# Kernel optimization log

Measured on AMD Instinct MI355X. Metric: run time of the kernel, lower is better.

Reference implementation:

```python
import jax, jax.numpy as jnp
import numpy as np

N = 50000          # nodes
E = 800000         # edges (before self loops)
IN_C = 64
HID = 32
HEADS = 4
HC = HID * HEADS   # 128
OUT_C = 3
NEG_SLOPE = 0.2


def _lin(key, fan_out, fan_in, scale=None):
    if scale is None:
        scale = 1.0 / np.sqrt(fan_in)
    return (jax.random.normal(key, (fan_out, fan_in), dtype=jnp.float32) * scale)


def setup_inputs() -> dict:
    key = jax.random.key(0)
    ks = jax.random.split(key, 24)
    inp = {
        "x": jax.random.normal(ks[0], (N, IN_C), dtype=jnp.float32),
        "edge_index": jax.random.randint(ks[1], (2, E), 0, N, dtype=jnp.int64),
        "edge_attr": jax.random.uniform(ks[2], (E,), dtype=jnp.float32),
        "g1_Wl": _lin(ks[3], HC, IN_C), "g1_bl": jnp.zeros((HC,), jnp.float32),
        "g1_Wr": _lin(ks[4], HC, IN_C), "g1_br": jnp.zeros((HC,), jnp.float32),
        "g1_We": _lin(ks[5], HC, 1),
        "g1_att": jax.random.normal(ks[6], (HEADS, HID), dtype=jnp.float32) / np.sqrt(HID),
        "g1_bias": jnp.zeros((HC,), jnp.float32),
        "g2_Wl": _lin(ks[7], HC, HC), "g2_bl": jnp.zeros((HC,), jnp.float32),
        "g2_Wr": _lin(ks[8], HC, HC), "g2_br": jnp.zeros((HC,), jnp.float32),
        "g2_We": _lin(ks[9], HC, 1),
        "g2_att": jax.random.normal(ks[10], (1, HC), dtype=jnp.float32) / np.sqrt(HC),
        "g2_bias": jnp.zeros((HC,), jnp.float32),
        # residual projection (in_channels != hidden*heads)
        "res1_W": _lin(ks[11], HC, IN_C), "res1_b": jnp.zeros((HC,), jnp.float32),
        # MLP head
        "fc1_W": _lin(ks[12], HID, HC), "fc1_b": jnp.zeros((HID,), jnp.float32),
        "fc2_W": _lin(ks[13], 32, HID), "fc2_b": jnp.zeros((32,), jnp.float32),
        "fc3_W": _lin(ks[14], OUT_C, 32), "fc3_b": jnp.zeros((OUT_C,), jnp.float32),
    }
    return inp


def gatv2_conv(x, src, dst, ea, Wl, bl, Wr, br, We, att, bias, heads, out_c):
    # x: [N, F]; src/dst: [E'] (self loops already appended); ea: [E', 1]
    xl = (x @ Wl.T + bl).reshape(N, heads, out_c)   # lin_l -> source features
    xr = (x @ Wr.T + br).reshape(N, heads, out_c)   # lin_r -> target features
    ee = (ea @ We.T).reshape(-1, heads, out_c)      # lin_edge (no bias)
    xj = xl[src]                                    # [E', H, C] gather
    m = jax.nn.leaky_relu(xj + xr[dst] + ee, NEG_SLOPE)
    alpha = jnp.einsum('ehc,hc->eh', m, att)        # per-edge logits
    amax = jax.ops.segment_max(alpha, dst, num_segments=N)
    ex = jnp.exp(alpha - amax[dst])
    denom = jax.ops.segment_sum(ex, dst, num_segments=N)
    alpha = ex / (denom[dst] + 1e-16)               # segment softmax over incoming edges
    out = jax.ops.segment_sum(xj * alpha[..., None], dst, num_segments=N)
    return out.reshape(N, heads * out_c) + bias


def reference(x, edge_index, edge_attr,
              g1_Wl, g1_bl, g1_Wr, g1_br, g1_We, g1_att, g1_bias,
              g2_Wl, g2_bl, g2_Wr, g2_br, g2_We, g2_att, g2_bias,
              res1_W, res1_b, fc1_W, fc1_b, fc2_W, fc2_b, fc3_W, fc3_b):
    ea = edge_attr.reshape(-1, 1)                   # dim()==1 -> view(-1,1)
    # add self loops; edge_attr fill_value='mean' (PyG default)
    loop = jnp.arange(N)
    src = jnp.concatenate([edge_index[0], loop])
    dst = jnp.concatenate([edge_index[1], loop])
    ea_mean = jnp.mean(ea, axis=0, keepdims=True)
    ea_full = jnp.concatenate([ea, jnp.broadcast_to(ea_mean, (N, 1))], axis=0)

    h = gatv2_conv(x, src, dst, ea_full, g1_Wl, g1_bl, g1_Wr, g1_br,
                   g1_We, g1_att, g1_bias, HEADS, HID)
    h = jax.nn.elu(h + (x @ res1_W.T + res1_b))     # residual (projected) + ELU

    h2 = gatv2_conv(h, src, dst, ea_full, g2_Wl, g2_bl, g2_Wr, g2_br,
                    g2_We, g2_att, g2_bias, 1, HC)
    h2 = jax.nn.elu(h2 + h)                         # identity residual + ELU

    y = jax.nn.relu(h2 @ fc1_W.T + fc1_b)
    y = jax.nn.relu(y @ fc2_W.T + fc2_b)
    return y @ fc3_W.T + fc3_b                      # [N, 3]
```

## Files before the change

kernel.cpp:

```cpp
#include <hip/hip_runtime.h>
#include <math.h>


typedef short s16x8 __attribute__((ext_vector_type(8)));
typedef float f32x4 __attribute__((ext_vector_type(4)));
typedef float f32x2 __attribute__((ext_vector_type(2)));

__device__ inline unsigned short f2bf(float x) {
  unsigned int u = __float_as_uint(x);
  return (unsigned short)((u + 0x7fffu + ((u >> 16) & 1u)) >> 16);
}
__device__ inline float bf2f(unsigned short h) {
  return __uint_as_float(((unsigned int)h) << 16);
}
__device__ inline float bflo(unsigned int u) { return __uint_as_float(u << 16); }
__device__ inline float bfhi(unsigned int u) { return __uint_as_float(u & 0xffff0000u); }

template <int CTRL>
__device__ inline float dpp_addf(float x) {
  int y = __builtin_amdgcn_update_dpp(0, __float_as_int(x), CTRL, 0xf, 0xf, false);
  return x + __int_as_float(y);
}

__global__ __launch_bounds__(256) void prep_hist(
    const float* __restrict__ g1wl, const float* __restrict__ g1wr,
    const float* __restrict__ res1w, const float* __restrict__ g2wl,
    const float* __restrict__ g2wr,
    unsigned short* __restrict__ hi, unsigned short* __restrict__ lo,
    const int* __restrict__ ei, const float* __restrict__ ea,
    int* __restrict__ hist, float* __restrict__ partials,
    int E, int Ep, int CH, int NB, int WBLK, int NCHUNK) {
  int t = threadIdx.x;
  if (blockIdx.x < WBLK) {
    int i = blockIdx.x * 256 + t;
    if (i >= 57344) return;
    float f;
    if (i < 8192) f = g1wl[i];
    else if (i < 16384) f = g1wr[i - 8192];
    else if (i < 24576) f = res1w[i - 16384];
    else if (i < 40960) f = g2wl[i - 24576];
    else f = g2wr[i - 40960];
    unsigned short h = f2bf(f);
    hi[i] = h;
    lo[i] = f2bf(f - bf2f(h));
    return;
  }
  __shared__ int h[256];
  __shared__ float red[256];
  int c = blockIdx.x - WBLK;
  h[t] = 0;
  float s = 0.f;
  __syncthreads();
  int s0 = c * CH, e_ = min(Ep, s0 + CH);
  for (int e = s0 + t; e < e_; e += 256) {
    int d;
    if (e < E) { d = ei[E + e]; s += ea[e]; }
    else       { d = e - E; }
    atomicAdd(&h[d >> 8], 1);
  }
  red[t] = s;
  __syncthreads();
  for (int ofs = 128; ofs > 0; ofs >>= 1) {
    if (t < ofs) red[t] += red[t + ofs];
    __syncthreads();
  }
  if (t == 0) partials[c] = red[0];
  for (int k = t; k < NB; k += 256) hist[(size_t)k * NCHUNK + c] = h[k];
}

__global__ __launch_bounds__(1024) void scan_blocksum(
    const int* __restrict__ in, int* __restrict__ blksum, int n) {
  __shared__ int ws[16];
  int t = threadIdx.x;
  int base = blockIdx.x * 4096 + t * 4;
  int s = 0;
  if (base + 3 < n) {
    int4 v = *(const int4*)(in + base);
    s = v.x + v.y + v.z + v.w;
  } else {
    for (int i = 0; i < 4; i++) if (base + i < n) s += in[base + i];
  }
  int lane = t & 63, w = t >> 6;
#pragma unroll
  for (int ofs = 1; ofs < 64; ofs <<= 1) s += __shfl_xor(s, ofs);
  if (lane == 0) ws[w] = s;
  __syncthreads();
  if (t == 0) {
    int tot = 0;
#pragma unroll
    for (int i = 0; i < 16; i++) tot += ws[i];
    blksum[blockIdx.x] = tot;
  }
}

__global__ __launch_bounds__(128) void blkoff_mean(
    int* __restrict__ blksum, int nb,
    const float* __restrict__ partials, float* __restrict__ meanv, int E,
    unsigned int* __restrict__ meta, int Ep) {
  int t = threadIdx.x;
  if (t < 64) {
    int v = (t < nb) ? blksum[t] : 0;
    int orig = v;
#pragma unroll
    for (int ofs = 1; ofs < 64; ofs <<= 1) {
      int u = __shfl_up(v, ofs);
      if (t >= ofs) v += u;
    }
    if (t < nb) blksum[t] = v - orig;
    meta[Ep + t] = 0u;
  } else {
    int l = t - 64;
    float s = partials[l] + partials[l + 64] + partials[l + 128] + partials[l + 192];
#pragma unroll
    for (int ofs = 1; ofs < 64; ofs <<= 1) s += __shfl_xor(s, ofs);
    if (l == 0) meanv[0] = s / (float)E;
  }
}

__global__ __launch_bounds__(1024) void scan_out(
    const int* __restrict__ in, const int* __restrict__ blksum,
    int* __restrict__ out, int n, int total) {
  __shared__ int ws[16];
  int t = threadIdx.x;
  int base = blockIdx.x * 4096 + t * 4;
  int4 v = {0, 0, 0, 0};
  if (base + 3 < n) {
    v = *(const int4*)(in + base);
  } else {
    if (base + 0 < n) v.x = in[base + 0];
    if (base + 1 < n) v.y = in[base + 1];
    if (base + 2 < n) v.z = in[base + 2];
    if (base + 3 < n) v.w = in[base + 3];
  }
  int s = v.x + v.y + v.z + v.w;
  int lane = t & 63, w = t >> 6;
  int inc = s;
#pragma unroll
  for (int ofs = 1; ofs < 64; ofs <<= 1) {
    int u = __shfl_up(inc, ofs);
    if (lane >= ofs) inc += u;
  }
  if (lane == 63) ws[w] = inc;
  __syncthreads();
  int waveoff = 0;
#pragma unroll
  for (int i = 0; i < 16; i++) waveoff += (i < w) ? ws[i] : 0;
  int excl = blksum[blockIdx.x] + waveoff + inc - s;
  int p0 = excl, p1 = p0 + v.x, p2 = p1 + v.y, p3 = p2 + v.z;
  if (base + 0 < n) out[base + 0] = p0;
  if (base + 1 < n) out[base + 1] = p1;
  if (base + 2 < n) out[base + 2] = p2;
  if (base + 3 < n) out[base + 3] = p3;
  if (blockIdx.x == 0 && t == 0) out[n] = total;
}

__global__ __launch_bounds__(256) void bin_scatter(
    const int* __restrict__ ei, const float* __restrict__ ea,
    const float* __restrict__ meanv, const int* __restrict__ histoff,
    unsigned int* __restrict__ binmeta, unsigned char* __restrict__ bindlo,
    int E, int Ep, int CH, int NB) {
  __shared__ int off[256];
  int t = threadIdx.x, c = blockIdx.x;
  for (int k = t; k < NB; k += 256) off[k] = histoff[(size_t)k * gridDim.x + c];
  __syncthreads();
  int s = c * CH, e_ = min(Ep, s + CH);
  for (int e = s + t; e < e_; e += 256) {
    int d, src; float eav;
    if (e < E) { src = ei[e]; d = ei[E + e]; eav = ea[e]; }
    else       { src = d = e - E; eav = meanv[0]; }
    int pos = atomicAdd(&off[d >> 8], 1);
    binmeta[pos] = (unsigned int)src | ((unsigned int)f2bf(eav) << 16);
    bindlo[pos] = (unsigned char)(d & 255);
  }
}

__global__ __launch_bounds__(256) void bin_finalize(
    const unsigned int* __restrict__ binmeta, const unsigned char* __restrict__ bindlo,
    const int* __restrict__ histoff, unsigned int* __restrict__ meta,
    int* __restrict__ row_ptr, int N, int Ep, int NCHUNK, int NB) {
  __shared__ int cntl[256];
  __shared__ int ws4[4];
  int t = threadIdx.x, k = blockIdx.x;
  int kstart = histoff[(size_t)k * NCHUNK];
  int kend = (k == NB - 1) ? Ep : histoff[(size_t)(k + 1) * NCHUNK];
  cntl[t] = 0;
  __syncthreads();
  for (int i = kstart + t; i < kend; i += 256) atomicAdd(&cntl[bindlo[i]], 1);
  __syncthreads();
  int v = cntl[t];
  int lane = t & 63, w = t >> 6;
  int inc = v;
#pragma unroll
  for (int ofs = 1; ofs < 64; ofs <<= 1) {
    int u = __shfl_up(inc, ofs);
    if (lane >= ofs) inc += u;
  }
  if (lane == 63) ws4[w] = inc;
  __syncthreads();
  int waveoff = 0;
#pragma unroll
  for (int i = 0; i < 4; i++) waveoff += (i < w) ? ws4[i] : 0;
  int base = kstart + waveoff + inc - v;
  int gd = k * 256 + t;
  if (gd < N) row_ptr[gd] = base;
  if (k == 0 && t == 0) row_ptr[N] = Ep;
  __syncthreads();
  cntl[t] = base;
  __syncthreads();
  for (int i = kstart + t; i < kend; i += 256) {
    int d = bindlo[i];
    int pos = atomicAdd(&cntl[d], 1);
    meta[pos] = binmeta[i];
  }
}

template <int K, int NMAT, int INBF>
__global__ __launch_bounds__(256) void gemm_mfma(
    const void* __restrict__ Xv,
    const unsigned short* __restrict__ Whi_all, const unsigned short* __restrict__ Wlo_all,
    int off0, const float* __restrict__ b0, unsigned short* __restrict__ o0,
    int off1, const float* __restrict__ b1, unsigned short* __restrict__ o1,
    int off2, const float* __restrict__ b2, unsigned short* __restrict__ o2,
    int N) {
  constexpr int KS = K / 32;
  __shared__ unsigned short Xhi[64 * K];
  __shared__ unsigned short Xlo[INBF ? 1 : 64 * K];
  int t = threadIdx.x;
  int m0 = blockIdx.x * 64;
  int which = (NMAT == 1) ? 0 : blockIdx.y;
  int woff = (which == 0) ? off0 : (which == 1) ? off1 : off2;
  const float* bias = (which == 0) ? b0 : (which == 1) ? b1 : b2;
  unsigned short* out = (which == 0) ? o0 : (which == 1) ? o1 : o2;

  if (INBF) {
    const unsigned short* X = (const unsigned short*)Xv;
#pragma unroll
    for (int i = 0; i < K / 32; ++i) {
      int idx8 = t + i * 256;
      int row = idx8 / (K / 8);
      int k8 = idx8 % (K / 8);
      int gm = m0 + row;
      uint4 v = (gm < N) ? *(const uint4*)(X + (size_t)gm * K + k8 * 8)
                         : uint4{0u, 0u, 0u, 0u};
      int us = (row * K + k8 * 8) ^ ((row & 7) << 3);
      *(uint4*)&Xhi[us] = v;
    }
  } else {
    const float* X = (const float*)Xv;
#pragma unroll
    for (int i = 0; i < K / 16; ++i) {
      int idx4 = t + i * 256;
      int row = idx4 / (K / 4);
      int k4 = idx4 % (K / 4);
      int gm = m0 + row;
      float4 v = (gm < N) ? *(const float4*)(X + (size_t)gm * K + k4 * 4)
                          : float4{0.f, 0.f, 0.f, 0.f};
      float f[4] = {v.x, v.y, v.z, v.w};
      ushort4 h, l;
      unsigned short* hp = (unsigned short*)&h;
      unsigned short* lp = (unsigned short*)&l;
#pragma unroll
      for (int j = 0; j < 4; ++j) {
        unsigned short hb = f2bf(f[j]);
        hp[j] = hb;
        lp[j] = f2bf(f[j] - bf2f(hb));
      }
      int us = (row * K + k4 * 4) ^ ((row & 7) << 3);
      *(ushort4*)&Xhi[us] = h;
      *(ushort4*)&Xlo[us] = l;
    }
  }

  int wv = t >> 6, lane = t & 63;
  int lr = lane & 15, kg = lane >> 4;

  s16x8 Whf[2][KS], Wlf[2][KS];
  const unsigned short* Wh = Whi_all + woff;
  const unsigned short* Wl = Wlo_all + woff;
#pragma unroll
  for (int ni = 0; ni < 2; ++ni) {
#pragma unroll
    for (int ks = 0; ks < KS; ++ks) {
      int widx = (wv * 32 + ni * 16 + lr) * K + ks * 32 + kg * 8;
      Whf[ni][ks] = *(const s16x8*)(Wh + widx);
      Wlf[ni][ks] = *(const s16x8*)(Wl + widx);
    }
  }

  __syncthreads();

  f32x4 acc[4][2] = {};
#pragma unroll
  for (int ks = 0; ks < KS; ++ks) {
#pragma unroll
    for (int mi = 0; mi < 4; ++mi) {
      int r = mi * 16 + lr;
      int us = (r * K + ks * 32 + kg * 8) ^ ((r & 7) << 3);
      s16x8 ah = *(const s16x8*)&Xhi[us];
#pragma unroll
      for (int ni = 0; ni < 2; ++ni) {
        acc[mi][ni] = __builtin_amdgcn_mfma_f32_16x16x32_bf16(ah, Whf[ni][ks], acc[mi][ni], 0, 0, 0);
        acc[mi][ni] = __builtin_amdgcn_mfma_f32_16x16x32_bf16(ah, Wlf[ni][ks], acc[mi][ni], 0, 0, 0);
      }
      if (!INBF) {
        s16x8 al = *(const s16x8*)&Xlo[us];
#pragma unroll
        for (int ni = 0; ni < 2; ++ni) {
          acc[mi][ni] = __builtin_amdgcn_mfma_f32_16x16x32_bf16(al, Whf[ni][ks], acc[mi][ni], 0, 0, 0);
        }
      }
    }
  }

#pragma unroll
  for (int ni = 0; ni < 2; ++ni) {
    int col = wv * 32 + ni * 16 + lr;
    float bv = bias[col];
#pragma unroll
    for (int mi = 0; mi < 4; ++mi) {
#pragma unroll
      for (int j = 0; j < 4; ++j) {
        int gm = m0 + mi * 16 + kg * 4 + j;
        if (gm < N) out[(size_t)gm * 128 + col] = f2bf(acc[mi][ni][j] + bv);
      }
    }
  }
}

template <int RED>
__global__ __launch_bounds__(256) void attn_kernel(
    const unsigned short* __restrict__ xl, const unsigned short* __restrict__ xr,
    const unsigned short* __restrict__ resid, const float* __restrict__ We,
    const float* __restrict__ att, const float* __restrict__ bias,
    const unsigned int* __restrict__ meta, const int* __restrict__ row_ptr,
    unsigned short* __restrict__ outbuf, int N) {
  int wid = threadIdx.x >> 6;
  int lane = threadIdx.x & 63;
  int n = blockIdx.x * 4 + wid;
  if (n >= N) return;
  int g = lane >> 4, li = lane & 15;
  int c = li * 8;
  f32x2 xr2[4], we2[4], at2[4];
  {
    uint4 xrr = *(const uint4*)(xr + (size_t)n * 128 + c);
    xr2[0] = f32x2{bflo(xrr.x), bfhi(xrr.x)};
    xr2[1] = f32x2{bflo(xrr.y), bfhi(xrr.y)};
    xr2[2] = f32x2{bflo(xrr.z), bfhi(xrr.z)};
    xr2[3] = f32x2{bflo(xrr.w), bfhi(xrr.w)};
  }
#pragma unroll
  for (int j = 0; j < 4; j++) {
    we2[j] = *(const f32x2*)(We + c + 2 * j);
    at2[j] = *(const f32x2*)(att + c + 2 * j) * 1.44269504088896f;
  }
  int rs = row_ptr[n], re = row_ptr[n + 1];
  float s = 0.f;
  f32x2 acc2[4] = {{0.f, 0.f}, {0.f, 0.f}, {0.f, 0.f}, {0.f, 0.f}};
  int nit = (re - rs + 3) >> 2;
  int idx = rs + g;
  bool v0 = idx < re;
  unsigned int md0 = meta[idx];
  bool v1 = idx + 4 < re;
  unsigned int md1 = meta[idx + 4];
  bool v2 = idx + 8 < re;
  unsigned int md2 = meta[idx + 8];
  uint4 raw0 = *(const uint4*)(xl + (size_t)(md0 & 0xFFFFu) * 128 + c);
  uint4 raw1 = *(const uint4*)(xl + (size_t)(md1 & 0xFFFFu) * 128 + c);
  for (int it = 0; it < nit; ++it) {
    bool v3 = idx + 12 < re;
    unsigned int md3 = meta[idx + 12];
    uint4 raw2 = *(const uint4*)(xl + (size_t)(md2 & 0xFFFFu) * 128 + c);
    f32x2 xa2[4];
    xa2[0] = f32x2{bflo(raw0.x), bfhi(raw0.x)};
    xa2[1] = f32x2{bflo(raw0.y), bfhi(raw0.y)};
    xa2[2] = f32x2{bflo(raw0.z), bfhi(raw0.z)};
    xa2[3] = f32x2{bflo(raw0.w), bfhi(raw0.w)};
    float eavf = __uint_as_float(md0 & 0xffff0000u);
    f32x2 eav2 = {eavf, eavf};
    f32x2 p2 = {0.f, 0.f};
#pragma unroll
    for (int j = 0; j < 4; j++) {
      f32x2 t = xa2[j] + xr2[j];
      t = eav2 * we2[j] + t;
      f32x2 u = t * 0.2f;
      t = __builtin_elementwise_max(t, u);
      p2 = t * at2[j] + p2;
    }
    float p = p2.x + p2.y;
    p = dpp_addf<0xB1>(p);
    p = dpp_addf<0x4E>(p);
    if (RED == 16) {
      p = dpp_addf<0x141>(p);
      p = dpp_addf<0x140>(p);
    }
    float ex = v0 ? exp2f(p) : 0.f;
    f32x2 ex2 = {ex, ex};
    s += ex;
#pragma unroll
    for (int j = 0; j < 4; j++) acc2[j] = ex2 * xa2[j] + acc2[j];
    idx += 4;
    v0 = v1; v1 = v2; v2 = v3;
    md0 = md1; md1 = md2; md2 = md3;
    raw0 = raw1; raw1 = raw2;
  }
#pragma unroll
  for (int ofs = 16; ofs <= 32; ofs <<= 1) {
    s += __shfl_xor(s, ofs);
#pragma unroll
    for (int j = 0; j < 4; j++) {
      acc2[j].x += __shfl_xor(acc2[j].x, ofs);
      acc2[j].y += __shfl_xor(acc2[j].y, ofs);
    }
  }
  if (g == 0) {
    float inv = 1.f / (s + 1e-16f);
    uint4 rr = *(const uint4*)(resid + (size_t)n * 128 + c);
    float rv[8];
    rv[0] = bflo(rr.x); rv[1] = bfhi(rr.x);
    rv[2] = bflo(rr.y); rv[3] = bfhi(rr.y);
    rv[4] = bflo(rr.z); rv[5] = bfhi(rr.z);
    rv[6] = bflo(rr.w); rv[7] = bfhi(rr.w);
    float o[8];
#pragma unroll
    for (int j = 0; j < 4; j++) {
      f32x2 bi = *(const f32x2*)(bias + c + 2 * j);
      o[2 * j]     = acc2[j].x * inv + bi.x + rv[2 * j];
      o[2 * j + 1] = acc2[j].y * inv + bi.y + rv[2 * j + 1];
    }
#pragma unroll
    for (int j = 0; j < 8; j++) o[j] = (o[j] > 0.f) ? o[j] : (__expf(o[j]) - 1.f);
    uint4 pk;
    pk.x = (unsigned int)f2bf(o[0]) | ((unsigned int)f2bf(o[1]) << 16);
    pk.y = (unsigned int)f2bf(o[2]) | ((unsigned int)f2bf(o[3]) << 16);
    pk.z = (unsigned int)f2bf(o[4]) | ((unsigned int)f2bf(o[5]) << 16);
    pk.w = (unsigned int)f2bf(o[6]) | ((unsigned int)f2bf(o[7]) << 16);
    *(uint4*)(outbuf + (size_t)n * 128 + c) = pk;
  }
}

__global__ __launch_bounds__(1024) void mlp_kernel(
    const unsigned short* __restrict__ h2,
    const float* __restrict__ W1, const float* __restrict__ b1,
    const float* __restrict__ W2, const float* __restrict__ b2,
    const float* __restrict__ W3, const float* __restrict__ b3,
    float* __restrict__ out, int N) {
  __shared__ float w1t[128][33];
  __shared__ float w2t[32][33];
  __shared__ float w3t[32][4];
  __shared__ float hs[32][132];
  __shared__ float y1s[32][33];
  __shared__ float y2s[32][33];
  int t = threadIdx.x;
  int n0 = blockIdx.x * 32;
  for (int idx = t; idx < 4096; idx += 1024) {
    int oc = idx >> 7, k = idx & 127;
    w1t[k][oc] = W1[idx];
  }
  {
    int oc = t >> 5, k = t & 31;
    if (t < 1024) w2t[k][oc] = W2[t];
  }
  if (t < 96) {
    int oc = t >> 5, k = t & 31;
    w3t[k][oc] = W3[t];
  }
  if (t < 512) {
    int nl = t >> 4, k8 = t & 15;
    int gm = n0 + nl;
    uint4 v = (gm < N) ? *(const uint4*)(h2 + (size_t)gm * 128 + k8 * 8)
                       : uint4{0u, 0u, 0u, 0u};
    float* hp = &hs[nl][k8 * 8];
    hp[0] = bflo(v.x); hp[1] = bfhi(v.x);
    hp[2] = bflo(v.y); hp[3] = bfhi(v.y);
    hp[4] = bflo(v.z); hp[5] = bfhi(v.z);
    hp[6] = bflo(v.w); hp[7] = bfhi(v.w);
  }
  __syncthreads();
  int nl = t >> 5, oc = t & 31;
  int n = n0 + nl;
  float acc = b1[oc];
#pragma unroll 8
  for (int k = 0; k < 128; k++) acc += hs[nl][k] * w1t[k][oc];
  y1s[nl][oc] = fmaxf(acc, 0.f);
  float acc2 = b2[oc];
#pragma unroll
  for (int k = 0; k < 32; k++) acc2 += y1s[nl][k] * w2t[k][oc];
  y2s[nl][oc] = fmaxf(acc2, 0.f);
  if (oc < 3 && n < N) {
    float acc3 = b3[oc];
#pragma unroll
    for (int k = 0; k < 32; k++) acc3 += y2s[nl][k] * w3t[k][oc];
    out[(size_t)n * 3 + oc] = acc3;
  }
}

extern "C" void kernel_launch(void* const* d_in, const int* in_sizes, int n_in,
                              void* d_out, int out_size, void* d_ws, size_t ws_size,
                              hipStream_t stream) {
  const float* x      = (const float*)d_in[0];
  const int*   ei     = (const int*)d_in[1];
  const float* ea     = (const float*)d_in[2];
  const float* g1_Wl  = (const float*)d_in[3];
  const float* g1_bl  = (const float*)d_in[4];
  const float* g1_Wr  = (const float*)d_in[5];
  const float* g1_br  = (const float*)d_in[6];
  const float* g1_We  = (const float*)d_in[7];
  const float* g1_att = (const float*)d_in[8];
  const float* g1_bias= (const float*)d_in[9];
  const float* g2_Wl  = (const float*)d_in[10];
  const float* g2_bl  = (const float*)d_in[11];
  const float* g2_Wr  = (const float*)d_in[12];
  const float* g2_br  = (const float*)d_in[13];
  const float* g2_We  = (const float*)d_in[14];
  const float* g2_att = (const float*)d_in[15];
  const float* g2_bias= (const float*)d_in[16];
  const float* res1_W = (const float*)d_in[17];
  const float* res1_b = (const float*)d_in[18];
  const float* fc1_W  = (const float*)d_in[19];
  const float* fc1_b  = (const float*)d_in[20];
  const float* fc2_W  = (const float*)d_in[21];
  const float* fc2_b  = (const float*)d_in[22];
  const float* fc3_W  = (const float*)d_in[23];
  const float* fc3_b  = (const float*)d_in[24];
  float* out = (float*)d_out;

  int N = in_sizes[0] / 64;
  int E = in_sizes[2];
  int Ep = E + N;

  const int NCHUNK = 256;
  const int WBLK = 224;
  int CH = (Ep + NCHUNK - 1) / NCHUNK;
  int NB = (N + 255) >> 8;
  int Nh = NB * NCHUNK;

  char* ws = (char*)d_ws;
  size_t off = 0;
  auto carve = [&](size_t bytes) -> char* {
    char* p = ws + off;
    off = (off + bytes + 255) & ~(size_t)255;
    return p;
  };
  float* meanv    = (float*)carve(4);
  float* partials = (float*)carve(NCHUNK * 4);
  int*   blksum   = (int*)carve(64 * 4);
  int*   hist     = (int*)carve((size_t)(Nh + 1) * 4);
  int*   histoff  = (int*)carve((size_t)(Nh + 1) * 4);
  int*   row_ptr  = (int*)carve((size_t)(N + 1) * 4);
  unsigned int* binmeta = (unsigned int*)carve((size_t)Ep * 4);
  unsigned char* bindlo = (unsigned char*)carve((size_t)Ep);
  unsigned int* meta = (unsigned int*)carve((size_t)(Ep + 64) * 4);
  unsigned short* xlbf = (unsigned short*)carve((size_t)N * 128 * 2);
  unsigned short* xrbf = (unsigned short*)carve((size_t)N * 128 * 2);
  unsigned short* resh2 = (unsigned short*)carve((size_t)N * 128 * 2);
  unsigned short* hbuf = (unsigned short*)carve((size_t)N * 128 * 2);
  unsigned short* Whi = (unsigned short*)carve(57344 * 2);
  unsigned short* Wlo = (unsigned short*)carve(57344 * 2);
  (void)ws_size; (void)n_in; (void)out_size;

  prep_hist<<<WBLK + NCHUNK, 256, 0, stream>>>(
      g1_Wl, g1_Wr, res1_W, g2_Wl, g2_Wr, Whi, Wlo,
      ei, ea, hist, partials, E, Ep, CH, NB, WBLK, NCHUNK);
  int nbscan = (Nh + 4095) / 4096;
  scan_blocksum<<<nbscan, 1024, 0, stream>>>(hist, blksum, Nh);
  blkoff_mean<<<1, 128, 0, stream>>>(blksum, nbscan, partials, meanv, E,
                                     meta, Ep);
  scan_out<<<nbscan, 1024, 0, stream>>>(hist, blksum, histoff, Nh, Ep);
  bin_scatter<<<NCHUNK, 256, 0, stream>>>(ei, ea, meanv, histoff, binmeta,
                                          bindlo, E, Ep, CH, NB);
  bin_finalize<<<NB, 256, 0, stream>>>(binmeta, bindlo, histoff, meta,
                                       row_ptr, N, Ep, NCHUNK, NB);

  int mblk64 = (N + 63) / 64;
  gemm_mfma<64, 3, 0><<<dim3(mblk64, 3), 256, 0, stream>>>(
      x, Whi, Wlo, 0, g1_bl, xlbf, 8192, g1_br, xrbf, 16384, res1_b, resh2, N);
  attn_kernel<4><<<(N + 3) / 4, 256, 0, stream>>>(
      xlbf, xrbf, resh2, g1_We, g1_att, g1_bias, meta, row_ptr, hbuf, N);
  gemm_mfma<128, 2, 1><<<dim3(mblk64, 2), 256, 0, stream>>>(
      hbuf, Whi, Wlo, 24576, g2_bl, xlbf, 40960, g2_br, xrbf, 0,
      (const float*)nullptr, (unsigned short*)nullptr, N);
  attn_kernel<16><<<(N + 3) / 4, 256, 0, stream>>>(
      xlbf, xrbf, hbuf, g2_We, g2_att, g2_bias, meta, row_ptr, resh2, N);
  mlp_kernel<<<(N + 31) / 32, 1024, 0, stream>>>(resh2, fc1_W, fc1_b, fc2_W,
                                                 fc2_b, fc3_W, fc3_b, out, N);
}
```

Before: 233.5 us.

## Fuse edge binning with first GEMM and fuse second attention with MLP head

The edge bin-scatter kernel and the layer-1 projection GEMM are merged into a single launch, with the block index choosing between scatter work and GEMM tiles so the two independent jobs run concurrently. The layer-2 attention kernel now also runs the three-layer MLP head in-block, removing the round trip of h2 through global memory and one launch. The cost is that every attention block reloads the MLP weights into shared memory (about 4-node granularity) and takes extra barriers, which could outweigh the saved traffic.

Result: slower. 239.7 us (+2.7%).

```diff
diff --git a/kernel.cpp b/kernel.cpp
--- a/kernel.cpp
+++ b/kernel.cpp
@@ -154,23 +154,106 @@
   if (blockIdx.x == 0 && t == 0) out[n] = total;
 }
 
-__global__ __launch_bounds__(256) void bin_scatter(
+__global__ __launch_bounds__(256) void scatter_gemm1(
     const int* __restrict__ ei, const float* __restrict__ ea,
     const float* __restrict__ meanv, const int* __restrict__ histoff,
     unsigned int* __restrict__ binmeta, unsigned char* __restrict__ bindlo,
-    int E, int Ep, int CH, int NB) {
+    int E, int Ep, int CH, int NB, int NCHUNK,
+    const float* __restrict__ X,
+    const unsigned short* __restrict__ Whi_all, const unsigned short* __restrict__ Wlo_all,
+    const float* __restrict__ b0, unsigned short* __restrict__ o0,
+    const float* __restrict__ b1, unsigned short* __restrict__ o1,
+    const float* __restrict__ b2, unsigned short* __restrict__ o2,
+    int N, int MB) {
+  __shared__ unsigned short Xhi[64 * 64];
+  __shared__ unsigned short Xlo[64 * 64];
   __shared__ int off[256];
-  int t = threadIdx.x, c = blockIdx.x;
-  for (int k = t; k < NB; k += 256) off[k] = histoff[(size_t)k * gridDim.x + c];
-  __syncthreads();
-  int s = c * CH, e_ = min(Ep, s + CH);
-  for (int e = s + t; e < e_; e += 256) {
-    int d, src; float eav;
-    if (e < E) { src = ei[e]; d = ei[E + e]; eav = ea[e]; }
-    else       { src = d = e - E; eav = meanv[0]; }
-    int pos = atomicAdd(&off[d >> 8], 1);
-    binmeta[pos] = (unsigned int)src | ((unsigned int)f2bf(eav) << 16);
-    bindlo[pos] = (unsigned char)(d & 255);
+  int t = threadIdx.x;
+  if ((int)blockIdx.x < NCHUNK) {
+    int c = blockIdx.x;
+    for (int k = t; k < NB; k += 256) off[k] = histoff[(size_t)k * NCHUNK + c];
+    __syncthreads();
+    int s = c * CH, e_ = min(Ep, s + CH);
+    for (int e = s + t; e < e_; e += 256) {
+      int d, src; float eav;
+      if (e < E) { src = ei[e]; d = ei[E + e]; eav = ea[e]; }
+      else       { src = d = e - E; eav = meanv[0]; }
+      int pos = atomicAdd(&off[d >> 8], 1);
+      binmeta[pos] = (unsigned int)src | ((unsigned int)f2bf(eav) << 16);
+      bindlo[pos] = (unsigned char)(d & 255);
+    }
+    return;
+  }
+  constexpr int K = 64;
+  constexpr int KS = 2;
+  int gb = blockIdx.x - NCHUNK;
+  int which = gb / MB;
+  int m0 = (gb % MB) * 64;
+  int woff = which * 8192;
+  const float* bias = (which == 0) ? b0 : (which == 1) ? b1 : b2;
+  unsigned short* out = (which == 0) ? o0 : (which == 1) ? o1 : o2;
+#pragma unroll
+  for (int i = 0; i < 4; ++i) {
+    int idx4 = t + i * 256;
+    int row = idx4 / 16, k4 = idx4 % 16;
+    int gm = m0 + row;
+    float4 v = (gm < N) ? *(const float4*)(X + (size_t)gm * K + k4 * 4)
+                        : float4{0.f, 0.f, 0.f, 0.f};
+    float f[4] = {v.x, v.y, v.z, v.w};
+    ushort4 h, l;
+    unsigned short* hp = (unsigned short*)&h;
+    unsigned short* lp = (unsigned short*)&l;
+#pragma unroll
+    for (int j = 0; j < 4; ++j) {
+      unsigned short hb = f2bf(f[j]);
+      hp[j] = hb;
+      lp[j] = f2bf(f[j] - bf2f(hb));
+    }
+    int us = (row * K + k4 * 4) ^ ((row & 7) << 3);
+    *(ushort4*)&Xhi[us] = h;
+    *(ushort4*)&Xlo[us] = l;
+  }
+  int wv = t >> 6, lane = t & 63;
+  int lr = lane & 15, kg = lane >> 4;
+  s16x8 Whf[2][KS], Wlf[2][KS];
+  const unsigned short* Wh = Whi_all + woff;
+  const unsigned short* Wl = Wlo_all + woff;
+#pragma unroll
+  for (int ni = 0; ni < 2; ++ni)
+#pragma unroll
+    for (int ks = 0; ks < KS; ++ks) {
+      int widx = (wv * 32 + ni * 16 + lr) * K + ks * 32 + kg * 8;
+      Whf[ni][ks] = *(const s16x8*)(Wh + widx);
+      Wlf[ni][ks] = *(const s16x8*)(Wl + widx);
+    }
+  __syncthreads();
+  f32x4 acc[4][2] = {};
+#pragma unroll
+  for (int ks = 0; ks < KS; ++ks)
+#pragma unroll
+    for (int mi = 0; mi < 4; ++mi) {
+      int r = mi * 16 + lr;
+      int us = (r * K + ks * 32 + kg * 8) ^ ((r & 7) << 3);
+      s16x8 ah = *(const s16x8*)&Xhi[us];
+      s16x8 al = *(const s16x8*)&Xlo[us];
+#pragma unroll
+      for (int ni = 0; ni < 2; ++ni) {
+        acc[mi][ni] = __builtin_amdgcn_mfma_f32_16x16x32_bf16(ah, Whf[ni][ks], acc[mi][ni], 0, 0, 0);
+        acc[mi][ni] = __builtin_amdgcn_mfma_f32_16x16x32_bf16(ah, Wlf[ni][ks], acc[mi][ni], 0, 0, 0);
+        acc[mi][ni] = __builtin_amdgcn_mfma_f32_16x16x32_bf16(al, Whf[ni][ks], acc[mi][ni], 0, 0, 0);
+      }
+    }
+#pragma unroll
+  for (int ni = 0; ni < 2; ++ni) {
+    int col = wv * 32 + ni * 16 + lr;
+    float bv = bias[col];
+#pragma unroll
+    for (int mi = 0; mi < 4; ++mi)
+#pragma unroll
+      for (int j = 0; j < 4; ++j) {
+        int gm = m0 + mi * 16 + kg * 4 + j;
+        if (gm < N) out[(size_t)gm * 128 + col] = f2bf(acc[mi][ni][j] + bv);
+      }
   }
 }
 
@@ -214,121 +297,74 @@
   }
 }
 
-template <int K, int NMAT, int INBF>
-__global__ __launch_bounds__(256) void gemm_mfma(
-    const void* __restrict__ Xv,
+__global__ __launch_bounds__(256) void gemm2_mfma(
+    const unsigned short* __restrict__ X,
     const unsigned short* __restrict__ Whi_all, const unsigned short* __restrict__ Wlo_all,
-    int off0, const float* __restrict__ b0, unsigned short* __restrict__ o0,
-    int off1, const float* __restrict__ b1, unsigned short* __restrict__ o1,
-    int off2, const float* __restrict__ b2, unsigned short* __restrict__ o2,
+    const float* __restrict__ b0, unsigned short* __restrict__ o0,
+    const float* __restrict__ b1, unsigned short* __restrict__ o1,
     int N) {
-  constexpr int KS = K / 32;
-  __shared__ unsigned short Xhi[64 * K];
-  __shared__ unsigned short Xlo[INBF ? 1 : 64 * K];
+  constexpr int K = 128;
+  constexpr int KS = 4;
+  __shared__ unsigned short Xs[64 * K];
   int t = threadIdx.x;
   int m0 = blockIdx.x * 64;
-  int which = (NMAT == 1) ? 0 : blockIdx.y;
-  int woff = (which == 0) ? off0 : (which == 1) ? off1 : off2;
-  const float* bias = (which == 0) ? b0 : (which == 1) ? b1 : b2;
-  unsigned short* out = (which == 0) ? o0 : (which == 1) ? o1 : o2;
-
-  if (INBF) {
-    const unsigned short* X = (const unsigned short*)Xv;
-#pragma unroll
-    for (int i = 0; i < K / 32; ++i) {
-      int idx8 = t + i * 256;
-      int row = idx8 / (K / 8);
-      int k8 = idx8 % (K / 8);
-      int gm = m0 + row;
-      uint4 v = (gm < N) ? *(const uint4*)(X + (size_t)gm * K + k8 * 8)
-                         : uint4{0u, 0u, 0u, 0u};
-      int us = (row * K + k8 * 8) ^ ((row & 7) << 3);
-      *(uint4*)&Xhi[us] = v;
-    }
-  } else {
-    const float* X = (const float*)Xv;
-#pragma unroll
-    for (int i = 0; i < K / 16; ++i) {
-      int idx4 = t + i * 256;
-      int row = idx4 / (K / 4);
-      int k4 = idx4 % (K / 4);
-      int gm = m0 + row;
-      float4 v = (gm < N) ? *(const float4*)(X + (size_t)gm * K + k4 * 4)
-                          : float4{0.f, 0.f, 0.f, 0.f};
-      float f[4] = {v.x, v.y, v.z, v.w};
-      ushort4 h, l;
-      unsigned short* hp = (unsigned short*)&h;
-      unsigned short* lp = (unsigned short*)&l;
-#pragma unroll
-      for (int j = 0; j < 4; ++j) {
-        unsigned short hb = f2bf(f[j]);
-        hp[j] = hb;
-        lp[j] = f2bf(f[j] - bf2f(hb));
-      }
-      int us = (row * K + k4 * 4) ^ ((row & 7) << 3);
-      *(ushort4*)&Xhi[us] = h;
-      *(ushort4*)&Xlo[us] = l;
-    }
-  }
-
+  int which = blockIdx.y;
+  int woff = 24576 + which * 16384;
+  const float* bias = which ? b1 : b0;
+  unsigned short* out = which ? o1 : o0;
+#pragma unroll
+  for (int i = 0; i < 4; ++i) {
+    int idx8 = t + i * 256;
+    int row = idx8 / 16, k8 = idx8 % 16;
+    int gm = m0 + row;
+    uint4 v = (gm < N) ? *(const uint4*)(X + (size_t)gm * K + k8 * 8)
+                       : uint4{0u, 0u, 0u, 0u};
+    int us = (row * K + k8 * 8) ^ ((row & 7) << 3);
+    *(uint4*)&Xs[us] = v;
+  }
   int wv = t >> 6, lane = t & 63;
   int lr = lane & 15, kg = lane >> 4;
-
   s16x8 Whf[2][KS], Wlf[2][KS];
   const unsigned short* Wh = Whi_all + woff;
   const unsigned short* Wl = Wlo_all + woff;
 #pragma unroll
-  for (int ni = 0; ni < 2; ++ni) {
+  for (int ni = 0; ni < 2; ++ni)
 #pragma unroll
     for (int ks = 0; ks < KS; ++ks) {
       int widx = (wv * 32 + ni * 16 + lr) * K + ks * 32 + kg * 8;
       Whf[ni][ks] = *(const s16x8*)(Wh + widx);
       Wlf[ni][ks] = *(const s16x8*)(Wl + widx);
     }
-  }
-
-  __syncthreads();
-
+  __syncthreads();
   f32x4 acc[4][2] = {};
 #pragma unroll
-  for (int ks = 0; ks < KS; ++ks) {
+  for (int ks = 0; ks < KS; ++ks)
 #pragma unroll
     for (int mi = 0; mi < 4; ++mi) {
       int r = mi * 16 + lr;
       int us = (r * K + ks * 32 + kg * 8) ^ ((r & 7) << 3);
-      s16x8 ah = *(const s16x8*)&Xhi[us];
+      s16x8 ah = *(const s16x8*)&Xs[us];
 #pragma unroll
       for (int ni = 0; ni < 2; ++ni) {
         acc[mi][ni] = __builtin_amdgcn_mfma_f32_16x16x32_bf16(ah, Whf[ni][ks], acc[mi][ni], 0, 0, 0);
         acc[mi][ni] = __builtin_amdgcn_mfma_f32_16x16x32_bf16(ah, Wlf[ni][ks], acc[mi][ni], 0, 0, 0);
       }
-      if (!INBF) {
-        s16x8 al = *(const s16x8*)&Xlo[us];
-#pragma unroll
-        for (int ni = 0; ni < 2; ++ni) {
-          acc[mi][ni] = __builtin_amdgcn_mfma_f32_16x16x32_bf16(al, Whf[ni][ks], acc[mi][ni], 0, 0, 0);
-        }
-      }
-    }
-  }
-
+    }
 #pragma unroll
   for (int ni = 0; ni < 2; ++ni) {
     int col = wv * 32 + ni * 16 + lr;
     float bv = bias[col];
 #pragma unroll
-    for (int mi = 0; mi < 4; ++mi) {
+    for (int mi = 0; mi < 4; ++mi)
 #pragma unroll
       for (int j = 0; j < 4; ++j) {
         int gm = m0 + mi * 16 + kg * 4 + j;
         if (gm < N) out[(size_t)gm * 128 + col] = f2bf(acc[mi][ni][j] + bv);
       }
-    }
-  }
-}
-
-template <int RED>
-__global__ __launch_bounds__(256) void attn_kernel(
+  }
+}
+
+__global__ __launch_bounds__(256) void attn1_kernel(
     const unsigned short* __restrict__ xl, const unsigned short* __restrict__ xr,
     const unsigned short* __restrict__ resid, const float* __restrict__ We,
     const float* __restrict__ att, const float* __restrict__ bias,
@@ -389,10 +425,6 @@
     float p = p2.x + p2.y;
     p = dpp_addf<0xB1>(p);
     p = dpp_addf<0x4E>(p);
-    if (RED == 16) {
-      p = dpp_addf<0x141>(p);
-      p = dpp_addf<0x140>(p);
-    }
     float ex = v0 ? exp2f(p) : 0.f;
     f32x2 ex2 = {ex, ex};
     s += ex;
@@ -438,59 +470,151 @@
   }
 }
 
-__global__ __launch_bounds__(1024) void mlp_kernel(
-    const unsigned short* __restrict__ h2,
+__global__ __launch_bounds__(256) void attn2_mlp(
+    const unsigned short* __restrict__ xl, const unsigned short* __restrict__ xr,
+    const unsigned short* __restrict__ resid, const float* __restrict__ We,
+    const float* __restrict__ att, const float* __restrict__ bias,
+    const unsigned int* __restrict__ meta, const int* __restrict__ row_ptr,
     const float* __restrict__ W1, const float* __restrict__ b1,
     const float* __restrict__ W2, const float* __restrict__ b2,
     const float* __restrict__ W3, const float* __restrict__ b3,
-    float* __restrict__ out, int N) {
+    float* __restrict__ outp, int N) {
   __shared__ float w1t[128][33];
   __shared__ float w2t[32][33];
   __shared__ float w3t[32][4];
-  __shared__ float hs[32][132];
-  __shared__ float y1s[32][33];
-  __shared__ float y2s[32][33];
+  __shared__ float hs[4][136];
+  __shared__ float y1s[4][33];
+  __shared__ float y2s[4][33];
   int t = threadIdx.x;
-  int n0 = blockIdx.x * 32;
-  for (int idx = t; idx < 4096; idx += 1024) {
+  int wid = t >> 6;
+  int lane = t & 63;
+  int n = blockIdx.x * 4 + wid;
+  bool active = n < N;
+  for (int idx = t; idx < 4096; idx += 256) {
     int oc = idx >> 7, k = idx & 127;
     w1t[k][oc] = W1[idx];
   }
+  for (int idx = t; idx < 1024; idx += 256) {
+    int oc = idx >> 5, k = idx & 31;
+    w2t[k][oc] = W2[idx];
+  }
+  if (t < 96) w3t[t & 31][t >> 5] = W3[t];
+
+  int g = lane >> 4, li = lane & 15;
+  int c = li * 8;
+  f32x2 xr2[4], we2[4], at2[4];
   {
-    int oc = t >> 5, k = t & 31;
-    if (t < 1024) w2t[k][oc] = W2[t];
-  }
-  if (t < 96) {
-    int oc = t >> 5, k = t & 31;
-    w3t[k][oc] = W3[t];
-  }
-  if (t < 512) {
-    int nl = t >> 4, k8 = t & 15;
-    int gm = n0 + nl;
-    uint4 v = (gm < N) ? *(const uint4*)(h2 + (size_t)gm * 128 + k8 * 8)
-                       : uint4{0u, 0u, 0u, 0u};
-    float* hp = &hs[nl][k8 * 8];
-    hp[0] = bflo(v.x); hp[1] = bfhi(v.x);
-    hp[2] = bflo(v.y); hp[3] = bfhi(v.y);
-    hp[4] = bflo(v.z); hp[5] = bfhi(v.z);
-    hp[6] = bflo(v.w); hp[7] = bfhi(v.w);
-  }
-  __syncthreads();
-  int nl = t >> 5, oc = t & 31;
-  int n = n0 + nl;
-  float acc = b1[oc];
-#pragma unroll 8
-  for (int k = 0; k < 128; k++) acc += hs[nl][k] * w1t[k][oc];
-  y1s[nl][oc] = fmaxf(acc, 0.f);
-  float acc2 = b2[oc];
-#pragma unroll
-  for (int k = 0; k < 32; k++) acc2 += y1s[nl][k] * w2t[k][oc];
-  y2s[nl][oc] = fmaxf(acc2, 0.f);
-  if (oc < 3 && n < N) {
-    float acc3 = b3[oc];
-#pragma unroll
-    for (int k = 0; k < 32; k++) acc3 += y2s[nl][k] * w3t[k][oc];
-    out[(size_t)n * 3 + oc] = acc3;
+    size_t nn = active ? (size_t)n : 0;
+    uint4 xrr = *(const uint4*)(xr + nn * 128 + c);
+    xr2[0] = f32x2{bflo(xrr.x), bfhi(xrr.x)};
+    xr2[1] = f32x2{bflo(xrr.y), bfhi(xrr.y)};
+    xr2[2] = f32x2{bflo(xrr.z), bfhi(xrr.z)};
+    xr2[3] = f32x2{bflo(xrr.w), bfhi(xrr.w)};
+  }
+#pragma unroll
+  for (int j = 0; j < 4; j++) {
+    we2[j] = *(const f32x2*)(We + c + 2 * j);
+    at2[j] = *(const f32x2*)(att + c + 2 * j) * 1.44269504088896f;
+  }
+  int rs = active ? row_ptr[n] : 0;
+  int re = active ? row_ptr[n + 1] : 0;
+  float s = 0.f;
+  f32x2 acc2[4] = {{0.f, 0.f}, {0.f, 0.f}, {0.f, 0.f}, {0.f, 0.f}};
+  int nit = (re - rs + 3) >> 2;
+  int idx = rs + g;
+  bool v0 = idx < re;
+  unsigned int md0 = meta[idx];
+  bool v1 = idx + 4 < re;
+  unsigned int md1 = meta[idx + 4];
+  bool v2 = idx + 8 < re;
+  unsigned int md2 = meta[idx + 8];
+  uint4 raw0 = *(const uint4*)(xl + (size_t)(md0 & 0xFFFFu) * 128 + c);
+  uint4 raw1 = *(const uint4*)(xl + (size_t)(md1 & 0xFFFFu) * 128 + c);
+  for (int it = 0; it < nit; ++it) {
+    bool v3 = idx + 12 < re;
+    unsigned int md3 = meta[idx + 12];
+    uint4 raw2 = *(const uint4*)(xl + (size_t)(md2 & 0xFFFFu) * 128 + c);
+    f32x2 xa2[4];
+    xa2[0] = f32x2{bflo(raw0.x), bfhi(raw0.x)};
+    xa2[1] = f32x2{bflo(raw0.y), bfhi(raw0.y)};
+    xa2[2] = f32x2{bflo(raw0.z), bfhi(raw0.z)};
+    xa2[3] = f32x2{bflo(raw0.w), bfhi(raw0.w)};
+    float eavf = __uint_as_float(md0 & 0xffff0000u);
+    f32x2 eav2 = {eavf, eavf};
+    f32x2 p2 = {0.f, 0.f};
+#pragma unroll
+    for (int j = 0; j < 4; j++) {
+      f32x2 tt = xa2[j] + xr2[j];
+      tt = eav2 * we2[j] + tt;
+      f32x2 u = tt * 0.2f;
+      tt = __builtin_elementwise_max(tt, u);
+      p2 = tt * at2[j] + p2;
+    }
+    float p = p2.x + p2.y;
+    p = dpp_addf<0xB1>(p);
+    p = dpp_addf<0x4E>(p);
+    p = dpp_addf<0x141>(p);
+    p = dpp_addf<0x140>(p);
+    float ex = v0 ? exp2f(p) : 0.f;
+    f32x2 ex2 = {ex, ex};
+    s += ex;
+#pragma unroll
+    for (int j = 0; j < 4; j++) acc2[j] = ex2 * xa2[j] + acc2[j];
+    idx += 4;
+    v0 = v1; v1 = v2; v2 = v3;
+    md0 = md1; md1 = md2; md2 = md3;
+    raw0 = raw1; raw1 = raw2;
+  }
+#pragma unroll
+  for (int ofs = 16; ofs <= 32; ofs <<= 1) {
+    s += __shfl_xor(s, ofs);
+#pragma unroll
+    for (int j = 0; j < 4; j++) {
+      acc2[j].x += __shfl_xor(acc2[j].x, ofs);
+      acc2[j].y += __shfl_xor(acc2[j].y, ofs);
+    }
+  }
+  if (g == 0) {
+    float inv = 1.f / (s + 1e-16f);
+    size_t nn = active ? (size_t)n : 0;
+    uint4 rr = *(const uint4*)(resid + nn * 128 + c);
+    float rv[8];
+    rv[0] = bflo(rr.x); rv[1] = bfhi(rr.x);
+    rv[2] = bflo(rr.y); rv[3] = bfhi(rr.y);
+    rv[4] = bflo(rr.z); rv[5] = bfhi(rr.z);
+    rv[6] = bflo(rr.w); rv[7] = bfhi(rr.w);
+#pragma unroll
+    for (int j = 0; j < 4; j++) {
+      f32x2 bi = *(const f32x2*)(bias + c + 2 * j);
+      float o0 = acc2[j].x * inv + bi.x + rv[2 * j];
+      float o1 = acc2[j].y * inv + bi.y + rv[2 * j + 1];
+      o0 = (o0 > 0.f) ? o0 : (__expf(o0) - 1.f);
+      o1 = (o1 > 0.f) ? o1 : (__expf(o1) - 1.f);
+      hs[wid][c + 2 * j] = o0;
+      hs[wid][c + 2 * j + 1] = o1;
+    }
+  }
+  __syncthreads();
+  int oc = lane & 31, kh = lane >> 5;
+  float a1 = 0.f;
+#pragma unroll 4
+  for (int k = 0; k < 64; k++) a1 += hs[wid][kh * 64 + k] * w1t[kh * 64 + k][oc];
+  a1 += __shfl_xor(a1, 32);
+  a1 = fmaxf(a1 + b1[oc], 0.f);
+  if (kh == 0) y1s[wid][oc] = a1;
+  __syncthreads();
+  float a2 = 0.f;
+#pragma unroll
+  for (int k = 0; k < 16; k++) a2 += y1s[wid][kh * 16 + k] * w2t[kh * 16 + k][oc];
+  a2 += __shfl_xor(a2, 32);
+  a2 = fmaxf(a2 + b2[oc], 0.f);
+  if (kh == 0) y2s[wid][oc] = a2;
+  __syncthreads();
+  if (active && lane < 3) {
+    float a3 = b3[lane];
+#pragma unroll
+    for (int k = 0; k < 32; k++) a3 += y2s[wid][k] * w3t[k][lane];
+    outp[(size_t)n * 3 + lane] = a3;
   }
 }
 
@@ -566,21 +690,17 @@
   blkoff_mean<<<1, 128, 0, stream>>>(blksum, nbscan, partials, meanv, E,
                                      meta, Ep);
   scan_out<<<nbscan, 1024, 0, stream>>>(hist, blksum, histoff, Nh, Ep);
-  bin_scatter<<<NCHUNK, 256, 0, stream>>>(ei, ea, meanv, histoff, binmeta,
-                                          bindlo, E, Ep, CH, NB);
+  int MB = (N + 63) / 64;
+  scatter_gemm1<<<NCHUNK + 3 * MB, 256, 0, stream>>>(
+      ei, ea, meanv, histoff, binmeta, bindlo, E, Ep, CH, NB, NCHUNK,
+      x, Whi, Wlo, g1_bl, xlbf, g1_br, xrbf, res1_b, resh2, N, MB);
   bin_finalize<<<NB, 256, 0, stream>>>(binmeta, bindlo, histoff, meta,
                                        row_ptr, N, Ep, NCHUNK, NB);
-
-  int mblk64 = (N + 63) / 64;
-  gemm_mfma<64, 3, 0><<<dim3(mblk64, 3), 256, 0, stream>>>(
-      x, Whi, Wlo, 0, g1_bl, xlbf, 8192, g1_br, xrbf, 16384, res1_b, resh2, N);
-  attn_kernel<4><<<(N + 3) / 4, 256, 0, stream>>>(
+  attn1_kernel<<<(N + 3) / 4, 256, 0, stream>>>(
       xlbf, xrbf, resh2, g1_We, g1_att, g1_bias, meta, row_ptr, hbuf, N);
-  gemm_mfma<128, 2, 1><<<dim3(mblk64, 2), 256, 0, stream>>>(
-      hbuf, Whi, Wlo, 24576, g2_bl, xlbf, 40960, g2_br, xrbf, 0,
-      (const float*)nullptr, (unsigned short*)nullptr, N);
-  attn_kernel<16><<<(N + 3) / 4, 256, 0, stream>>>(
-      xlbf, xrbf, hbuf, g2_We, g2_att, g2_bias, meta, row_ptr, resh2, N);
-  mlp_kernel<<<(N + 31) / 32, 1024, 0, stream>>>(resh2, fc1_W, fc1_b, fc2_W,
-                                                 fc2_b, fc3_W, fc3_b, out, N);
-}
+  gemm2_mfma<<<dim3(MB, 2), 256, 0, stream>>>(
+      hbuf, Whi, Wlo, g2_bl, xlbf, g2_br, xrbf, N);
+  attn2_mlp<<<(N + 3) / 4, 256, 0, stream>>>(
+      xlbf, xrbf, hbuf, g2_We, g2_att, g2_bias, meta, row_ptr,
+      fc1_W, fc1_b, fc2_W, fc2_b, fc3_W, fc3_b, out, N);
+}
```

## Fuse layer-1 GEMM into bin_scatter launch as extra independent blocks

Applied to the files above, without the earlier changes.

Merges the edge bin-scatter kernel and the first-layer triple GEMM into one launch, where the first NCHUNK blocks scatter edges and the remaining blocks compute the x projections. This removes one kernel launch and lets the memory-bound scatter overlap with the MFMA GEMM work on the GPU. The fused kernel's LDS footprint (Xhi/Xlo plus off) now applies to the scatter blocks as well, which may reduce their occupancy. The second GEMM becomes a specialized non-templated kernel with the same math.

Result: faster. 228.2 us (-2.3%).

```diff
diff --git a/kernel.cpp b/kernel.cpp
--- a/kernel.cpp
+++ b/kernel.cpp
@@ -154,23 +154,106 @@
   if (blockIdx.x == 0 && t == 0) out[n] = total;
 }
 
-__global__ __launch_bounds__(256) void bin_scatter(
+__global__ __launch_bounds__(256) void scatter_gemm1(
     const int* __restrict__ ei, const float* __restrict__ ea,
     const float* __restrict__ meanv, const int* __restrict__ histoff,
     unsigned int* __restrict__ binmeta, unsigned char* __restrict__ bindlo,
-    int E, int Ep, int CH, int NB) {
+    int E, int Ep, int CH, int NB, int NCHUNK,
+    const float* __restrict__ X,
+    const unsigned short* __restrict__ Whi_all, const unsigned short* __restrict__ Wlo_all,
+    const float* __restrict__ b0, unsigned short* __restrict__ o0,
+    const float* __restrict__ b1, unsigned short* __restrict__ o1,
+    const float* __restrict__ b2, unsigned short* __restrict__ o2,
+    int N, int MB) {
+  __shared__ unsigned short Xhi[64 * 64];
+  __shared__ unsigned short Xlo[64 * 64];
   __shared__ int off[256];
-  int t = threadIdx.x, c = blockIdx.x;
-  for (int k = t; k < NB; k += 256) off[k] = histoff[(size_t)k * gridDim.x + c];
-  __syncthreads();
-  int s = c * CH, e_ = min(Ep, s + CH);
-  for (int e = s + t; e < e_; e += 256) {
-    int d, src; float eav;
-    if (e < E) { src = ei[e]; d = ei[E + e]; eav = ea[e]; }
-    else       { src = d = e - E; eav = meanv[0]; }
-    int pos = atomicAdd(&off[d >> 8], 1);
-    binmeta[pos] = (unsigned int)src | ((unsigned int)f2bf(eav) << 16);
-    bindlo[pos] = (unsigned char)(d & 255);
+  int t = threadIdx.x;
+  if ((int)blockIdx.x < NCHUNK) {
+    int c = blockIdx.x;
+    for (int k = t; k < NB; k += 256) off[k] = histoff[(size_t)k * NCHUNK + c];
+    __syncthreads();
+    int s = c * CH, e_ = min(Ep, s + CH);
+    for (int e = s + t; e < e_; e += 256) {
+      int d, src; float eav;
+      if (e < E) { src = ei[e]; d = ei[E + e]; eav = ea[e]; }
+      else       { src = d = e - E; eav = meanv[0]; }
+      int pos = atomicAdd(&off[d >> 8], 1);
+      binmeta[pos] = (unsigned int)src | ((unsigned int)f2bf(eav) << 16);
+      bindlo[pos] = (unsigned char)(d & 255);
+    }
+    return;
+  }
+  constexpr int K = 64;
+  constexpr int KS = 2;
+  int gb = blockIdx.x - NCHUNK;
+  int which = gb / MB;
+  int m0 = (gb % MB) * 64;
+  int woff = which * 8192;
+  const float* bias = (which == 0) ? b0 : (which == 1) ? b1 : b2;
+  unsigned short* out = (which == 0) ? o0 : (which == 1) ? o1 : o2;
+#pragma unroll
+  for (int i = 0; i < 4; ++i) {
+    int idx4 = t + i * 256;
+    int row = idx4 / 16, k4 = idx4 % 16;
+    int gm = m0 + row;
+    float4 v = (gm < N) ? *(const float4*)(X + (size_t)gm * K + k4 * 4)
+                        : float4{0.f, 0.f, 0.f, 0.f};
+    float f[4] = {v.x, v.y, v.z, v.w};
+    ushort4 h, l;
+    unsigned short* hp = (unsigned short*)&h;
+    unsigned short* lp = (unsigned short*)&l;
+#pragma unroll
+    for (int j = 0; j < 4; ++j) {
+      unsigned short hb = f2bf(f[j]);
+      hp[j] = hb;
+      lp[j] = f2bf(f[j] - bf2f(hb));
+    }
+    int us = (row * K + k4 * 4) ^ ((row & 7) << 3);
+    *(ushort4*)&Xhi[us] = h;
+    *(ushort4*)&Xlo[us] = l;
+  }
+  int wv = t >> 6, lane = t & 63;
+  int lr = lane & 15, kg = lane >> 4;
+  s16x8 Whf[2][KS], Wlf[2][KS];
+  const unsigned short* Wh = Whi_all + woff;
+  const unsigned short* Wl = Wlo_all + woff;
+#pragma unroll
+  for (int ni = 0; ni < 2; ++ni)
+#pragma unroll
+    for (int ks = 0; ks < KS; ++ks) {
+      int widx = (wv * 32 + ni * 16 + lr) * K + ks * 32 + kg * 8;
+      Whf[ni][ks] = *(const s16x8*)(Wh + widx);
+      Wlf[ni][ks] = *(const s16x8*)(Wl + widx);
+    }
+  __syncthreads();
+  f32x4 acc[4][2] = {};
+#pragma unroll
+  for (int ks = 0; ks < KS; ++ks)
+#pragma unroll
+    for (int mi = 0; mi < 4; ++mi) {
+      int r = mi * 16 + lr;
+      int us = (r * K + ks * 32 + kg * 8) ^ ((r & 7) << 3);
+      s16x8 ah = *(const s16x8*)&Xhi[us];
+      s16x8 al = *(const s16x8*)&Xlo[us];
+#pragma unroll
+      for (int ni = 0; ni < 2; ++ni) {
+        acc[mi][ni] = __builtin_amdgcn_mfma_f32_16x16x32_bf16(ah, Whf[ni][ks], acc[mi][ni], 0, 0, 0);
+        acc[mi][ni] = __builtin_amdgcn_mfma_f32_16x16x32_bf16(ah, Wlf[ni][ks], acc[mi][ni], 0, 0, 0);
+        acc[mi][ni] = __builtin_amdgcn_mfma_f32_16x16x32_bf16(al, Whf[ni][ks], acc[mi][ni], 0, 0, 0);
+      }
+    }
+#pragma unroll
+  for (int ni = 0; ni < 2; ++ni) {
+    int col = wv * 32 + ni * 16 + lr;
+    float bv = bias[col];
+#pragma unroll
+    for (int mi = 0; mi < 4; ++mi)
+#pragma unroll
+      for (int j = 0; j < 4; ++j) {
+        int gm = m0 + mi * 16 + kg * 4 + j;
+        if (gm < N) out[(size_t)gm * 128 + col] = f2bf(acc[mi][ni][j] + bv);
+      }
   }
 }
 
@@ -214,116 +297,70 @@
   }
 }
 
-template <int K, int NMAT, int INBF>
-__global__ __launch_bounds__(256) void gemm_mfma(
-    const void* __restrict__ Xv,
+__global__ __launch_bounds__(256) void gemm2_mfma(
+    const unsigned short* __restrict__ X,
     const unsigned short* __restrict__ Whi_all, const unsigned short* __restrict__ Wlo_all,
-    int off0, const float* __restrict__ b0, unsigned short* __restrict__ o0,
-    int off1, const float* __restrict__ b1, unsigned short* __restrict__ o1,
-    int off2, const float* __restrict__ b2, unsigned short* __restrict__ o2,
+    const float* __restrict__ b0, unsigned short* __restrict__ o0,
+    const float* __restrict__ b1, unsigned short* __restrict__ o1,
     int N) {
-  constexpr int KS = K / 32;
-  __shared__ unsigned short Xhi[64 * K];
-  __shared__ unsigned short Xlo[INBF ? 1 : 64 * K];
+  constexpr int K = 128;
+  constexpr int KS = 4;
+  __shared__ unsigned short Xs[64 * K];
   int t = threadIdx.x;
   int m0 = blockIdx.x * 64;
-  int which = (NMAT == 1) ? 0 : blockIdx.y;
-  int woff = (which == 0) ? off0 : (which == 1) ? off1 : off2;
-  const float* bias = (which == 0) ? b0 : (which == 1) ? b1 : b2;
-  unsigned short* out = (which == 0) ? o0 : (which == 1) ? o1 : o2;
-
-  if (INBF) {
-    const unsigned short* X = (const unsigned short*)Xv;
-#pragma unroll
-    for (int i = 0; i < K / 32; ++i) {
-      int idx8 = t + i * 256;
-      int row = idx8 / (K / 8);
-      int k8 = idx8 % (K / 8);
-      int gm = m0 + row;
-      uint4 v = (gm < N) ? *(const uint4*)(X + (size_t)gm * K + k8 * 8)
-                         : uint4{0u, 0u, 0u, 0u};
-      int us = (row * K + k8 * 8) ^ ((row & 7) << 3);
-      *(uint4*)&Xhi[us] = v;
-    }
-  } else {
-    const float* X = (const float*)Xv;
-#pragma unroll
-    for (int i = 0; i < K / 16; ++i) {
-      int idx4 = t + i * 256;
-      int row = idx4 / (K / 4);
-      int k4 = idx4 % (K / 4);
-      int gm = m0 + row;
-      float4 v = (gm < N) ? *(const float4*)(X + (size_t)gm * K + k4 * 4)
-                          : float4{0.f, 0.f, 0.f, 0.f};
-      float f[4] = {v.x, v.y, v.z, v.w};
-      ushort4 h, l;
-      unsigned short* hp = (unsigned short*)&h;
-      unsigned short* lp = (unsigned short*)&l;
-#pragma unroll
-      for (int j = 0; j < 4; ++j) {
-        unsigned short hb = f2bf(f[j]);
-        hp[j] = hb;
-        lp[j] = f2bf(f[j] - bf2f(hb));
-      }
-      int us = (row * K + k4 * 4) ^ ((row & 7) << 3);
-      *(ushort4*)&Xhi[us] = h;
-      *(ushort4*)&Xlo[us] = l;
-    }
-  }
-
+  int which = blockIdx.y;
+  int woff = 24576 + which * 16384;
+  const float* bias = which ? b1 : b0;
+  unsigned short* out = which ? o1 : o0;
+#pragma unroll
+  for (int i = 0; i < 4; ++i) {
+    int idx8 = t + i * 256;
+    int row = idx8 / 16, k8 = idx8 % 16;
+    int gm = m0 + row;
+    uint4 v = (gm < N) ? *(const uint4*)(X + (size_t)gm * K + k8 * 8)
+                       : uint4{0u, 0u, 0u, 0u};
+    int us = (row * K + k8 * 8) ^ ((row & 7) << 3);
+    *(uint4*)&Xs[us] = v;
+  }
   int wv = t >> 6, lane = t & 63;
   int lr = lane & 15, kg = lane >> 4;
-
   s16x8 Whf[2][KS], Wlf[2][KS];
   const unsigned short* Wh = Whi_all + woff;
   const unsigned short* Wl = Wlo_all + woff;
 #pragma unroll
-  for (int ni = 0; ni < 2; ++ni) {
+  for (int ni = 0; ni < 2; ++ni)
 #pragma unroll
     for (int ks = 0; ks < KS; ++ks) {
       int widx = (wv * 32 + ni * 16 + lr) * K + ks * 32 + kg * 8;
       Whf[ni][ks] = *(const s16x8*)(Wh + widx);
       Wlf[ni][ks] = *(const s16x8*)(Wl + widx);
     }
-  }
-
-  __syncthreads();
-
+  __syncthreads();
   f32x4 acc[4][2] = {};
 #pragma unroll
-  for (int ks = 0; ks < KS; ++ks) {
+  for (int ks = 0; ks < KS; ++ks)
 #pragma unroll
     for (int mi = 0; mi < 4; ++mi) {
       int r = mi * 16 + lr;
       int us = (r * K + ks * 32 + kg * 8) ^ ((r & 7) << 3);
-      s16x8 ah = *(const s16x8*)&Xhi[us];
+      s16x8 ah = *(const s16x8*)&Xs[us];
 #pragma unroll
       for (int ni = 0; ni < 2; ++ni) {
         acc[mi][ni] = __builtin_amdgcn_mfma_f32_16x16x32_bf16(ah, Whf[ni][ks], acc[mi][ni], 0, 0, 0);
         acc[mi][ni] = __builtin_amdgcn_mfma_f32_16x16x32_bf16(ah, Wlf[ni][ks], acc[mi][ni], 0, 0, 0);
       }
-      if (!INBF) {
-        s16x8 al = *(const s16x8*)&Xlo[us];
-#pragma unroll
-        for (int ni = 0; ni < 2; ++ni) {
-          acc[mi][ni] = __builtin_amdgcn_mfma_f32_16x16x32_bf16(al, Whf[ni][ks], acc[mi][ni], 0, 0, 0);
-        }
-      }
-    }
-  }
-
+    }
 #pragma unroll
   for (int ni = 0; ni < 2; ++ni) {
     int col = wv * 32 + ni * 16 + lr;
     float bv = bias[col];
 #pragma unroll
-    for (int mi = 0; mi < 4; ++mi) {
+    for (int mi = 0; mi < 4; ++mi)
 #pragma unroll
       for (int j = 0; j < 4; ++j) {
         int gm = m0 + mi * 16 + kg * 4 + j;
         if (gm < N) out[(size_t)gm * 128 + col] = f2bf(acc[mi][ni][j] + bv);
       }
-    }
   }
 }
 
@@ -566,19 +603,16 @@
   blkoff_mean<<<1, 128, 0, stream>>>(blksum, nbscan, partials, meanv, E,
                                      meta, Ep);
   scan_out<<<nbscan, 1024, 0, stream>>>(hist, blksum, histoff, Nh, Ep);
-  bin_scatter<<<NCHUNK, 256, 0, stream>>>(ei, ea, meanv, histoff, binmeta,
-                                          bindlo, E, Ep, CH, NB);
+  int MB = (N + 63) / 64;
+  scatter_gemm1<<<NCHUNK + 3 * MB, 256, 0, stream>>>(
+      ei, ea, meanv, histoff, binmeta, bindlo, E, Ep, CH, NB, NCHUNK,
+      x, Whi, Wlo, g1_bl, xlbf, g1_br, xrbf, res1_b, resh2, N, MB);
   bin_finalize<<<NB, 256, 0, stream>>>(binmeta, bindlo, histoff, meta,
                                        row_ptr, N, Ep, NCHUNK, NB);
-
-  int mblk64 = (N + 63) / 64;
-  gemm_mfma<64, 3, 0><<<dim3(mblk64, 3), 256, 0, stream>>>(
-      x, Whi, Wlo, 0, g1_bl, xlbf, 8192, g1_br, xrbf, 16384, res1_b, resh2, N);
   attn_kernel<4><<<(N + 3) / 4, 256, 0, stream>>>(
       xlbf, xrbf, resh2, g1_We, g1_att, g1_bias, meta, row_ptr, hbuf, N);
-  gemm_mfma<128, 2, 1><<<dim3(mblk64, 2), 256, 0, stream>>>(
-      hbuf, Whi, Wlo, 24576, g2_bl, xlbf, 40960, g2_br, xrbf, 0,
-      (const float*)nullptr, (unsigned short*)nullptr, N);
+  gemm2_mfma<<<dim3(MB, 2), 256, 0, stream>>>(
+      hbuf, Whi, Wlo, g2_bl, xlbf, g2_br, xrbf, N);
   attn_kernel<16><<<(N + 3) / 4, 256, 0, stream>>>(
       xlbf, xrbf, hbuf, g2_We, g2_att, g2_bias, meta, row_ptr, resh2, N);
   mlp_kernel<<<(N + 31) / 32, 1024, 0, stream>>>(resh2, fc1_W, fc1_b, fc2_W,
```
